# Kernel tuning notes

Measured on AMD Instinct MI355X. Metric: run time of the kernel, lower is better.

Reference implementation:

```python
import jax, jax.numpy as jnp
import numpy as np

FUTURE_K = 16
NEG_BIG = -1e9  # matches masked softmax semantics (invalid slots get exactly 0 weight in fp32)


def setup_inputs() -> dict:
    key = jax.random.key(0)
    hidden_states = jax.random.normal(key, (2, 4096, 1024), dtype=jnp.float32)
    return {"hidden_states": hidden_states}


def reference(hidden_states) -> jnp.ndarray:
    # Windowed future attention: for each position t, attend over the next
    # FUTURE_K hidden states (t+1 .. t+k), masked at the sequence end.
    B, S, H = hidden_states.shape
    k = FUTURE_K
    # pad on the right so every window is full-length
    x_padded = jnp.pad(hidden_states, ((0, 0), (0, k), (0, 0)))  # (B, S+k, H)
    t = jnp.arange(S)
    gidx = t[:, None] + 1 + jnp.arange(k)[None, :]               # (S, k) global indices
    windows = x_padded[:, gidx]                                   # (B, S, k, H)
    valid = gidx < S                                              # (S, k)
    # per-window dot-product scores, masked softmax over window slots
    scores = jnp.einsum('bth,btjh->btj', hidden_states, windows)  # (B, S, k)
    scores = jnp.where(valid[None], scores, NEG_BIG)
    weights = jax.nn.softmax(scores, axis=-1)
    # rows with no valid future (last positions) -> zero summary (torch nan_to_num)
    weights = jnp.where(valid[None], weights, 0.0)
    summary = jnp.einsum('btj,btjh->bth', weights, windows)       # (B, S, H)
    return summary
```

## Files before the change

kernel.cpp:

```cpp
#include <hip/hip_runtime.h>


typedef float f32x4 __attribute__((ext_vector_type(4)));
typedef unsigned int u32;
typedef u32 u32x4 __attribute__((ext_vector_type(4)));
typedef short bf16x8 __attribute__((ext_vector_type(8)));

namespace {
constexpr int kB = 2, kS = 4096, kH = 1024;
constexpr int kWaves = 8;
constexpr int kTilesT = 16;
constexpr int kBlocks = kB * kS / kTilesT;
constexpr int kXCD = 8;
constexpr int kCPX = kBlocks / kXCD;
constexpr int kHW = kH / kWaves;
}

__device__ __forceinline__ u32 f32u(float x){ return __builtin_bit_cast(u32, x); }
__device__ __forceinline__ float uf32(u32 x){ return __builtin_bit_cast(float, x); }
__device__ __forceinline__ u32 pkbf(float a, float b){ return (f32u(b)&0xFFFF0000u)|(f32u(a)>>16); }

struct Frag2 { bf16x8 hi, lo; };
__device__ __forceinline__ Frag2 split2(float4 u, float4 v) {
  float fu[8] = {u.x,u.y,u.z,u.w,v.x,v.y,v.z,v.w};
  u32 hw[4], lw[4];
#pragma unroll
  for (int i = 0; i < 4; ++i) {
    float a = fu[2*i], b = fu[2*i+1];
    u32 ua = f32u(a), ub = f32u(b);
    hw[i] = (ub & 0xFFFF0000u) | (ua >> 16);
    float la = a - uf32(ua & 0xFFFF0000u);
    float lb = b - uf32(ub & 0xFFFF0000u);
    lw[i] = (f32u(lb) & 0xFFFF0000u) | (f32u(la) >> 16);
  }
  Frag2 r;
  u32x4 h = {hw[0],hw[1],hw[2],hw[3]}, l = {lw[0],lw[1],lw[2],lw[3]};
  r.hi = __builtin_bit_cast(bf16x8, h);
  r.lo = __builtin_bit_cast(bf16x8, l);
  return r;
}

#define MFMA(A,B,C) __builtin_amdgcn_mfma_f32_16x16x32_bf16((A),(B),(C),0,0,0)

__global__ __launch_bounds__(512, 4)
void fenc_mfma(const float* __restrict__ x, float* __restrict__ out) {
  __shared__ f32x4 red[kWaves][2][64];
  const int lane = (int)(threadIdx.x & 63), wid = (int)(threadIdx.x >> 6);
  const int g = lane >> 4, c = lane & 15;

  const int xcd = (int)(blockIdx.x % kXCD);
  const int j   = (int)(blockIdx.x / kXCD);
  const int vb  = xcd * kCPX + (j % 32) * 2 + (j / 32);
  const int t0g = vb * kTilesT;
  const int b   = t0g / kS, t0 = t0g % kS;
  const float* __restrict__ xb = x + (size_t)b*kS*kH;
  float* __restrict__ ob = out + (size_t)b*kS*kH;
  const int hw0 = kHW * wid;

  const int ra = (t0 + 1 + c  < kS) ? (t0 + 1 + c)  : (kS - 1);
  const int rb = (t0 + 17 + c < kS) ? (t0 + 17 + c) : (kS - 1);
  const float* qp  = xb + (size_t)(t0 + c)*kH + hw0;
  const float* kpa = xb + (size_t)ra*kH + hw0;
  const float* kpb = xb + (size_t)rb*kH + hw0;

  f32x4 aHH = {0.f,0.f,0.f,0.f}, aHL = aHH, aLH = aHH;
  f32x4 bHH = aHH, bHL = aHH, bLH = aHH;
  __builtin_amdgcn_s_setprio(1);
#pragma unroll
  for (int ks = 0; ks < 4; ++ks) {
    const int off = ks*32 + g*8;
    float4 q0 = *(const float4*)(qp  + off), q1 = *(const float4*)(qp  + off + 4);
    float4 a0 = *(const float4*)(kpa + off), a1 = *(const float4*)(kpa + off + 4);
    float4 b0 = *(const float4*)(kpb + off), b1 = *(const float4*)(kpb + off + 4);
    Frag2 fq = split2(q0, q1), fa = split2(a0, a1), fb = split2(b0, b1);
    aHH = MFMA(fa.hi, fq.hi, aHH);
    aHL = MFMA(fa.hi, fq.lo, aHL);
    aLH = MFMA(fa.lo, fq.hi, aLH);
    bHH = MFMA(fb.hi, fq.hi, bHH);
    bHL = MFMA(fb.hi, fq.lo, bHL);
    bLH = MFMA(fb.lo, fq.hi, bLH);
  }
  __builtin_amdgcn_s_setprio(0);
  f32x4 accA = (aHH + aHL) + aLH;
  f32x4 accB = (bHH + bHL) + bLH;

  const float* vrow[8];
#pragma unroll
  for (int i = 0; i < 8; ++i) {
    const int rv = t0 + 1 + 8*g + i;
    vrow[i] = xb + (size_t)((rv < kS) ? rv : (kS - 1))*kH + hw0 + c;
  }

  red[wid][0][lane] = accA;
  red[wid][1][lane] = accB;
  __syncthreads();
#pragma unroll
  for (int w = 0; w < kWaves; ++w) {
    if (w != wid) {
      accA += red[w][0][lane];
      accB += red[w][1][lane];
    }
  }

  float p[2][4];
  float vmax = -1e30f;
#pragma unroll
  for (int T = 0; T < 2; ++T)
#pragma unroll
    for (int r = 0; r < 4; ++r) {
      const int w = 16*T + 4*g + r;
      const bool val = (w >= c) && (w < c + 16) && (t0 + 1 + w < kS);
      const float sv = val ? (T ? accB[r] : accA[r]) : -1e30f;
      p[T][r] = sv;
      vmax = fmaxf(vmax, sv);
    }
  vmax = fmaxf(vmax, __shfl_xor(vmax, 16, 64));
  vmax = fmaxf(vmax, __shfl_xor(vmax, 32, 64));
  float psum = 0.f;
#pragma unroll
  for (int T = 0; T < 2; ++T)
#pragma unroll
    for (int r = 0; r < 4; ++r) {
      const int w = 16*T + 4*g + r;
      const bool val = (w >= c) && (w < c + 16) && (t0 + 1 + w < kS);
      const float e = val ? __expf(p[T][r] - vmax) : 0.f;
      p[T][r] = e;
      psum += e;
    }
  psum += __shfl_xor(psum, 16, 64);
  psum += __shfl_xor(psum, 32, 64);
  const float inv = (psum > 0.f) ? (1.f / psum) : 0.f;
#pragma unroll
  for (int T = 0; T < 2; ++T)
#pragma unroll
    for (int r = 0; r < 4; ++r) p[T][r] *= inv;

  const int se = (g & 1)*32 + c, so = se + 16;
  float slot[8];
#pragma unroll
  for (int r = 0; r < 4; ++r) {
    const float e0 = __shfl(p[0][r], se, 64), e1 = __shfl(p[1][r], se, 64);
    const float o0 = __shfl(p[0][r], so, 64), o1 = __shfl(p[1][r], so, 64);
    slot[r]     = (g >> 1) ? e1 : e0;
    slot[4 + r] = (g >> 1) ? o1 : o0;
  }
  u32x4 pw = { pkbf(slot[0],slot[1]), pkbf(slot[2],slot[3]),
               pkbf(slot[4],slot[5]), pkbf(slot[6],slot[7]) };
  const bf16x8 pa = __builtin_bit_cast(bf16x8, pw);

  f32x4 o[8];
  __builtin_amdgcn_s_setprio(1);
#pragma unroll
  for (int nt = 0; nt < 8; ++nt) {
    float vf[8];
#pragma unroll
    for (int i = 0; i < 8; ++i) vf[i] = vrow[i][16*nt];
    u32x4 vw = { pkbf(vf[0],vf[1]), pkbf(vf[2],vf[3]),
                 pkbf(vf[4],vf[5]), pkbf(vf[6],vf[7]) };
    const bf16x8 vfrag = __builtin_bit_cast(bf16x8, vw);
    f32x4 z = {0.f,0.f,0.f,0.f};
    o[nt] = MFMA(pa, vfrag, z);
  }
  __builtin_amdgcn_s_setprio(0);

  float* orow[4];
#pragma unroll
  for (int r = 0; r < 4; ++r)
    orow[r] = ob + (size_t)(t0 + 4*g + r)*kH + hw0 + c;
#pragma unroll
  for (int nt = 0; nt < 8; ++nt)
#pragma unroll
    for (int r = 0; r < 4; ++r)
      __builtin_nontemporal_store(o[nt][r], &orow[r][16*nt]);
}

extern "C" void kernel_launch(void* const* d_in, const int* in_sizes, int n_in,
                              void* d_out, int out_size, void* d_ws, size_t ws_size,
                              hipStream_t stream) {
  const float* x = (const float*)d_in[0];
  float* out = (float*)d_out;
  hipLaunchKernelGGL(fenc_mfma, dim3(kBlocks), dim3(512), 0, stream, x, out);
}
```

Measured before the change: 25.54 us.

## Stage bf16 key rows in swizzled LDS and reuse them for the value MFMA

During the score phase each wave now packs its loaded key rows to bf16 and writes them into a per-wave, XOR-swizzled shared-memory tile. The value-accumulation MFMA reads its B fragments from this tile instead of issuing eight strided global loads per lane per n-tile. The intent is to remove the redundant second global read of the window rows. The block-to-tile mapping is also simplified to a plain contiguous per-XCD order. The cost is 64 KB of LDS per block, which limits occupancy, plus scalar 16-bit LDS reads whose bank-conflict behaviour depends on the swizzle.

Result: faster. 24.30 us, median of 2 (-4.9%).

```diff
diff --git a/kernel.cpp b/kernel.cpp
--- a/kernel.cpp
+++ b/kernel.cpp
@@ -12,7 +12,6 @@
 constexpr int kTilesT = 16;
 constexpr int kBlocks = kB * kS / kTilesT;
 constexpr int kXCD = 8;
-constexpr int kCPX = kBlocks / kXCD;
 constexpr int kHW = kH / kWaves;
 }
 
@@ -45,12 +44,11 @@
 __global__ __launch_bounds__(512, 4)
 void fenc_mfma(const float* __restrict__ x, float* __restrict__ out) {
   __shared__ f32x4 red[kWaves][2][64];
+  __shared__ __align__(16) unsigned short kst[kWaves][32 * 128];
   const int lane = (int)(threadIdx.x & 63), wid = (int)(threadIdx.x >> 6);
   const int g = lane >> 4, c = lane & 15;
 
-  const int xcd = (int)(blockIdx.x % kXCD);
-  const int j   = (int)(blockIdx.x / kXCD);
-  const int vb  = xcd * kCPX + (j % 32) * 2 + (j / 32);
+  const int vb  = (int)(blockIdx.x % kXCD)*(kBlocks/kXCD) + (int)(blockIdx.x / kXCD);
   const int t0g = vb * kTilesT;
   const int b   = t0g / kS, t0 = t0g % kS;
   const float* __restrict__ xb = x + (size_t)b*kS*kH;
@@ -62,6 +60,10 @@
   const float* qp  = xb + (size_t)(t0 + c)*kH + hw0;
   const float* kpa = xb + (size_t)ra*kH + hw0;
   const float* kpb = xb + (size_t)rb*kH + hw0;
+  unsigned short* ks_base = &kst[wid][0];
+
+  const int wA = c,      xA = ((wA & 7) << 3) ^ ((wA >> 3) << 4);
+  const int wB = 16 + c, xB = ((wB & 7) << 3) ^ ((wB >> 3) << 4);
 
   f32x4 aHH = {0.f,0.f,0.f,0.f}, aHL = aHH, aLH = aHH;
   f32x4 bHH = aHH, bHL = aHH, bLH = aHH;
@@ -72,6 +74,12 @@
     float4 q0 = *(const float4*)(qp  + off), q1 = *(const float4*)(qp  + off + 4);
     float4 a0 = *(const float4*)(kpa + off), a1 = *(const float4*)(kpa + off + 4);
     float4 b0 = *(const float4*)(kpb + off), b1 = *(const float4*)(kpb + off + 4);
+
+    u32x4 pkA = { pkbf(a0.x,a0.y), pkbf(a0.z,a0.w), pkbf(a1.x,a1.y), pkbf(a1.z,a1.w) };
+    u32x4 pkB = { pkbf(b0.x,b0.y), pkbf(b0.z,b0.w), pkbf(b1.x,b1.y), pkbf(b1.z,b1.w) };
+    *(u32x4*)(ks_base + wA*128 + (off ^ xA)) = pkA;
+    *(u32x4*)(ks_base + wB*128 + (off ^ xB)) = pkB;
+
     Frag2 fq = split2(q0, q1), fa = split2(a0, a1), fb = split2(b0, b1);
     aHH = MFMA(fa.hi, fq.hi, aHH);
     aHL = MFMA(fa.hi, fq.lo, aHL);
@@ -83,13 +91,6 @@
   __builtin_amdgcn_s_setprio(0);
   f32x4 accA = (aHH + aHL) + aLH;
   f32x4 accB = (bHH + bHL) + bLH;
-
-  const float* vrow[8];
-#pragma unroll
-  for (int i = 0; i < 8; ++i) {
-    const int rv = t0 + 1 + 8*g + i;
-    vrow[i] = xb + (size_t)((rv < kS) ? rv : (kS - 1))*kH + hw0 + c;
-  }
 
   red[wid][0][lane] = accA;
   red[wid][1][lane] = accB;
@@ -152,11 +153,18 @@
   __builtin_amdgcn_s_setprio(1);
 #pragma unroll
   for (int nt = 0; nt < 8; ++nt) {
-    float vf[8];
+    const int m = 16*nt + c;
+    u32 vwj[4];
 #pragma unroll
-    for (int i = 0; i < 8; ++i) vf[i] = vrow[i][16*nt];
-    u32x4 vw = { pkbf(vf[0],vf[1]), pkbf(vf[2],vf[3]),
-                 pkbf(vf[4],vf[5]), pkbf(vf[6],vf[7]) };
+    for (int jj = 0; jj < 4; ++jj) {
+      const int w0 = 8*g + 2*jj, w1 = w0 + 1;
+      const int x0 = (((w0 & 7) << 3) ^ (g << 4));
+      const int x1 = (((w1 & 7) << 3) ^ (g << 4));
+      const u32 lo = ks_base[w0*128 + (m ^ x0)];
+      const u32 hi = ks_base[w1*128 + (m ^ x1)];
+      vwj[jj] = lo | (hi << 16);
+    }
+    u32x4 vw = { vwj[0], vwj[1], vwj[2], vwj[3] };
     const bf16x8 vfrag = __builtin_bit_cast(bf16x8, vw);
     f32x4 z = {0.f,0.f,0.f,0.f};
     o[nt] = MFMA(pa, vfrag, z);
```
